# Performance work log

Hardware: AMD Instinct MI355X
Metric: run time of the kernel (lower is better)

## Reference

```python
import jax, jax.numpy as jnp
import numpy as np

TOP_K = 2


def setup_inputs() -> dict:
    key = jax.random.key(0)
    k1, k2, k3, k4, k5 = jax.random.split(key, 5)
    H, F, E = 1024, 2048, 8
    B, S = 2, 1024
    return {
        "hidden_states": jax.random.normal(k1, (B, S, H), dtype=jnp.float32),
        "gate_w": jax.random.normal(k2, (E, H), dtype=jnp.float32) * (1.0 / np.sqrt(H)),
        "w1": jax.random.normal(k3, (E, F, H), dtype=jnp.float32) * (1.0 / np.sqrt(H)),
        "w2": jax.random.normal(k4, (E, H, F), dtype=jnp.float32) * (1.0 / np.sqrt(F)),
        "w3": jax.random.normal(k5, (E, F, H), dtype=jnp.float32) * (1.0 / np.sqrt(H)),
    }


def reference(hidden_states, gate_w, w1, w2, w3):
    B, S, H = hidden_states.shape
    E = gate_w.shape[0]
    x = hidden_states.reshape(-1, H)  # [T, H]

    # Router: softmax in float32, top-k, renormalize (exact Mixtral math)
    router_logits = x @ gate_w.T  # [T, E]
    probs = jax.nn.softmax(router_logits.astype(jnp.float32), axis=-1)
    routing_weights, selected = jax.lax.top_k(probs, TOP_K)  # [T, K]
    routing_weights = routing_weights / routing_weights.sum(axis=-1, keepdims=True)
    routing_weights = routing_weights.astype(x.dtype)

    # Per-token combine weight for each expert: [T, E]
    combine = (jax.nn.one_hot(selected, E, dtype=x.dtype) * routing_weights[..., None]).sum(axis=1)

    # Dense grouped expert SwiGLU MLP (zero combine weight for unselected experts
    # makes this strictly equivalent to the gathered/dispatched computation)
    h = jnp.einsum('th,efh->etf', x, w1)   # [E, T, F]
    g = jnp.einsum('th,efh->etf', x, w3)   # [E, T, F]
    mid = jax.nn.silu(h) * g               # SwiGLU
    expert_out = jnp.einsum('etf,ehf->eth', mid, w2)  # [E, T, H]
    out = jnp.einsum('eth,te->th', expert_out, combine)  # weighted combine

    return out.reshape(B, S, H), router_logits
```

## Files before the change

### kernel.cpp

```cpp
#include <hip/hip_runtime.h>
#include <hip/hip_bf16.h>
#include <math.h>

#define H 1024
#define FF 2048
#define E 8
#define T 2048
#define NSLOT (2*T)
#define SLOT_PAD 128

#define WCONV_BLKS 12288
#define XCONV_BLKS 512
#define ROUTER_BLKS T
#define K1_BLKS (WCONV_BLKS + XCONV_BLKS + ROUTER_BLKS)

typedef __attribute__((ext_vector_type(8))) short s16x8;
typedef __attribute__((ext_vector_type(4))) float f32x4;
typedef __attribute__((ext_vector_type(4))) unsigned int u32x4;

static __device__ __forceinline__ unsigned short f2bf(float f) {
    union { float f; unsigned u; } v; v.f = f;
    unsigned r = v.u + 0x7fff + ((v.u >> 16) & 1);
    return (unsigned short)(r >> 16);
}
static __device__ __forceinline__ float bf2f(unsigned short s) {
    union { unsigned u; float f; } v; v.u = ((unsigned)s) << 16;
    return v.f;
}
static __device__ __forceinline__ unsigned pack2(float a, float b) {
    return (unsigned)f2bf(a) | ((unsigned)f2bf(b) << 16);
}

typedef __attribute__((address_space(3))) unsigned int lds_uint;
typedef const __attribute__((address_space(1))) unsigned int glob_uint;
static __device__ __forceinline__ void gl_lds16(const void* g, void* l) {
    __builtin_amdgcn_global_load_lds((glob_uint*)g, (lds_uint*)l, 16, 0, 0);
}

static __device__ __forceinline__ void expert_range(const int* __restrict__ counts,
                                                    int e, int& off, int& cnt) {
    int acc = 0;
    #pragma unroll
    for (int i = 0; i < E; ++i) {
        int c = counts[i];
        if (i < e) acc += c;
        if (i == e) cnt = c;
    }
    off = acc;
}

__global__ __launch_bounds__(256) void prep_kernel(
    const float* __restrict__ x, const float* __restrict__ gw,
    const float* __restrict__ w1, const float* __restrict__ w3,
    const float* __restrict__ w2,
    unsigned short* __restrict__ w1b, unsigned short* __restrict__ w3b,
    unsigned short* __restrict__ w2b, unsigned short* __restrict__ xb,
    float* __restrict__ logits_out, int* __restrict__ top_id,
    float* __restrict__ top_w, int* __restrict__ counts)
{
    int b = blockIdx.x;
    int tid = threadIdx.x;
    if (b < WCONV_BLKS + XCONV_BLKS) {
        const float* s; unsigned short* d; size_t i;
        if (b < WCONV_BLKS) {
            int r = b >> 12;
            s = (r == 0) ? w1 : (r == 1) ? w3 : w2;
            d = (r == 0) ? w1b : (r == 1) ? w3b : w2b;
            i = ((size_t)(b & 4095) * 256 + tid) * 16;
        } else {
            s = x; d = xb;
            i = ((size_t)(b - WCONV_BLKS) * 256 + tid) * 16;
        }
        f32x4 a0 = __builtin_nontemporal_load((const f32x4*)(s + i));
        f32x4 a1 = __builtin_nontemporal_load((const f32x4*)(s + i + 4));
        f32x4 a2 = __builtin_nontemporal_load((const f32x4*)(s + i + 8));
        f32x4 a3 = __builtin_nontemporal_load((const f32x4*)(s + i + 12));
        u32x4 r0, r1;
        r0.x = pack2(a0.x, a0.y); r0.y = pack2(a0.z, a0.w);
        r0.z = pack2(a1.x, a1.y); r0.w = pack2(a1.z, a1.w);
        r1.x = pack2(a2.x, a2.y); r1.y = pack2(a2.z, a2.w);
        r1.z = pack2(a3.x, a3.y); r1.w = pack2(a3.z, a3.w);
        *(u32x4*)(d + i) = r0;
        *(u32x4*)(d + i + 8) = r1;
        return;
    }
    int t = b - (WCONV_BLKS + XCONV_BLKS);
    int e = tid >> 5;
    int l32 = tid & 31;
    const float* xr = x + (size_t)t * H;
    const float* gr = gw + (size_t)e * H;
    float s = 0.f;
    for (int h = l32; h < H; h += 32) s += xr[h] * gr[h];
    for (int off = 16; off; off >>= 1) s += __shfl_down(s, off, 32);
    __shared__ float lg[E];
    if (l32 == 0) lg[e] = s;
    __syncthreads();
    if (tid < E) logits_out[(size_t)t * E + tid] = lg[tid];
    if (tid == 0) {
        int i1 = 0; float b1 = lg[0];
        for (int i = 1; i < E; ++i) if (lg[i] > b1) { b1 = lg[i]; i1 = i; }
        int i2 = -1; float b2 = -INFINITY;
        for (int i = 0; i < E; ++i) if (i != i1 && lg[i] > b2) { b2 = lg[i]; i2 = i; }
        float p2 = expf(b2 - b1);
        float inv = 1.f / (1.f + p2);
        top_id[2*t]   = i1;  top_id[2*t+1] = i2;
        top_w[2*t]    = inv; top_w[2*t+1]  = p2 * inv;
        atomicAdd(&counts[i1], 1);
        atomicAdd(&counts[i2], 1);
    }
}

__global__ __launch_bounds__(256) void assign_kernel(
    const int* __restrict__ top_id, const int* __restrict__ counts,
    int* __restrict__ cursors, int* __restrict__ top_pos,
    int* __restrict__ slot_token)
{
    int t = blockIdx.x * 256 + threadIdx.x;
    if (t >= T) return;
    int offs[E];
    {
        int acc = 0;
        #pragma unroll
        for (int i = 0; i < E; ++i) { offs[i] = acc; acc += counts[i]; }
    }
    #pragma unroll
    for (int k = 0; k < 2; ++k) {
        int e = top_id[2*t + k];
        int p = offs[e] + atomicAdd(&cursors[e], 1);
        top_pos[2*t + k] = p;
        slot_token[p] = t;
    }
}

__global__ __launch_bounds__(256) void gemm1_kernel(
    const unsigned short* __restrict__ xb, const int* __restrict__ slot_token,
    const unsigned short* __restrict__ w1b, const unsigned short* __restrict__ w3b,
    const int* __restrict__ counts, unsigned short* __restrict__ mid)
{
    int e = blockIdx.z;
    int off, cnt;
    expert_range(counts, e, off, cnt);
    int m0 = blockIdx.y * 128;
    if (m0 >= cnt) return;
    int f0 = blockIdx.x * 64;

    __shared__ __align__(16) unsigned short sx[128 * 64];
    __shared__ __align__(16) unsigned short s1[64 * 64];
    __shared__ __align__(16) unsigned short s3[64 * 64];

    int tid = threadIdx.x;
    int wv = tid >> 6, ln = tid & 63;
    int quad = ln >> 4, l16 = ln & 15;
    int wm = wv & 1, wn = wv >> 1;
    int xor7 = l16 & 7;

    const unsigned short* xsrc[4]; unsigned short* xdst[4];
    #pragma unroll
    for (int j = 0; j < 4; ++j) {
        int row = wv * 32 + j * 8 + (ln >> 3);
        int slot = off + m0 + row;
        if (m0 + row >= cnt) slot = off;
        int tok = slot_token[slot];
        int cl = (ln & 7) ^ (row & 7);
        xsrc[j] = xb + (size_t)tok * H + cl * 8;
        xdst[j] = &sx[(wv * 32 + j * 8) * 64];
    }
    const unsigned short *w1s[2], *w3s[2]; unsigned short *d1[2], *d3[2];
    #pragma unroll
    for (int j = 0; j < 2; ++j) {
        int row = wv * 16 + j * 8 + (ln >> 3);
        int cl = (ln & 7) ^ (row & 7);
        w1s[j] = w1b + ((size_t)e * FF + f0 + row) * H + cl * 8;
        w3s[j] = w3b + ((size_t)e * FF + f0 + row) * H + cl * 8;
        d1[j] = &s1[(wv * 16 + j * 8) * 64];
        d3[j] = &s3[(wv * 16 + j * 8) * 64];
    }

    f32x4 acc1[4][2], acc3[4][2];
    #pragma unroll
    for (int i = 0; i < 4; ++i)
        #pragma unroll
        for (int j = 0; j < 2; ++j) {
            acc1[i][j] = (f32x4){0.f, 0.f, 0.f, 0.f};
            acc3[i][j] = (f32x4){0.f, 0.f, 0.f, 0.f};
        }

    for (int k0 = 0; k0 < H; k0 += 64) {
        #pragma unroll
        for (int j = 0; j < 4; ++j) gl_lds16(xsrc[j] + k0, xdst[j]);
        #pragma unroll
        for (int j = 0; j < 2; ++j) { gl_lds16(w1s[j] + k0, d1[j]); gl_lds16(w3s[j] + k0, d3[j]); }
        __syncthreads();
        #pragma unroll
        for (int ks = 0; ks < 2; ++ks) {
            int cph = ((quad + 4 * ks) ^ xor7) << 3;
            s16x8 a[4], b1v[2], b3v[2];
            #pragma unroll
            for (int i = 0; i < 4; ++i)
                a[i] = *(const s16x8*)&sx[(wm * 64 + i * 16 + l16) * 64 + cph];
            #pragma unroll
            for (int j = 0; j < 2; ++j) {
                b1v[j] = *(const s16x8*)&s1[(wn * 32 + j * 16 + l16) * 64 + cph];
                b3v[j] = *(const s16x8*)&s3[(wn * 32 + j * 16 + l16) * 64 + cph];
            }
            #pragma unroll
            for (int i = 0; i < 4; ++i)
                #pragma unroll
                for (int j = 0; j < 2; ++j) {
                    acc1[i][j] = __builtin_amdgcn_mfma_f32_16x16x32_bf16(a[i], b1v[j], acc1[i][j], 0, 0, 0);
                    acc3[i][j] = __builtin_amdgcn_mfma_f32_16x16x32_bf16(a[i], b3v[j], acc3[i][j], 0, 0, 0);
                }
        }
        __syncthreads();
    }

    #pragma unroll
    for (int i = 0; i < 4; ++i) {
        #pragma unroll
        for (int r = 0; r < 4; ++r) {
            int row = wm * 64 + i * 16 + quad * 4 + r;
            if (m0 + row < cnt) {
                size_t base = (size_t)(off + m0 + row) * FF + f0 + wn * 32;
                #pragma unroll
                for (int j = 0; j < 2; ++j) {
                    float h = acc1[i][j][r];
                    float g = acc3[i][j][r];
                    float v = h / (1.f + __expf(-h)) * g;
                    mid[base + j * 16 + l16] = f2bf(v);
                }
            }
        }
    }
}

__global__ __launch_bounds__(256) void gemm2_kernel(
    const unsigned short* __restrict__ mid, const unsigned short* __restrict__ w2b,
    const int* __restrict__ counts, unsigned short* __restrict__ y)
{
    int e = blockIdx.z;
    int off, cnt;
    expert_range(counts, e, off, cnt);
    int m0 = blockIdx.y * 128;
    if (m0 >= cnt) return;
    int n0 = blockIdx.x * 64;

    __shared__ __align__(16) unsigned short sa[128 * 64];
    __shared__ __align__(16) unsigned short sb[64 * 64];

    int tid = threadIdx.x;
    int wv = tid >> 6, ln = tid & 63;
    int quad = ln >> 4, l16 = ln & 15;
    int wm = wv & 1, wn = wv >> 1;
    int xor7 = l16 & 7;

    const unsigned short* asrc[4]; unsigned short* adst[4];
    #pragma unroll
    for (int j = 0; j < 4; ++j) {
        int row = wv * 32 + j * 8 + (ln >> 3);
        int cl = (ln & 7) ^ (row & 7);
        asrc[j] = mid + (size_t)(off + m0 + row) * FF + cl * 8;
        adst[j] = &sa[(wv * 32 + j * 8) * 64];
    }
    const unsigned short* bsrc[2]; unsigned short* bdst[2];
    #pragma unroll
    for (int j = 0; j < 2; ++j) {
        int row = wv * 16 + j * 8 + (ln >> 3);
        int cl = (ln & 7) ^ (row & 7);
        bsrc[j] = w2b + ((size_t)e * H + n0 + row) * FF + cl * 8;
        bdst[j] = &sb[(wv * 16 + j * 8) * 64];
    }

    f32x4 acc[4][2];
    #pragma unroll
    for (int i = 0; i < 4; ++i)
        #pragma unroll
        for (int j = 0; j < 2; ++j) acc[i][j] = (f32x4){0.f, 0.f, 0.f, 0.f};

    for (int k0 = 0; k0 < FF; k0 += 64) {
        #pragma unroll
        for (int j = 0; j < 4; ++j) gl_lds16(asrc[j] + k0, adst[j]);
        #pragma unroll
        for (int j = 0; j < 2; ++j) gl_lds16(bsrc[j] + k0, bdst[j]);
        __syncthreads();
        #pragma unroll
        for (int ks = 0; ks < 2; ++ks) {
            int cph = ((quad + 4 * ks) ^ xor7) << 3;
            s16x8 a[4], b[2];
            #pragma unroll
            for (int i = 0; i < 4; ++i)
                a[i] = *(const s16x8*)&sa[(wm * 64 + i * 16 + l16) * 64 + cph];
            #pragma unroll
            for (int j = 0; j < 2; ++j)
                b[j] = *(const s16x8*)&sb[(wn * 32 + j * 16 + l16) * 64 + cph];
            #pragma unroll
            for (int i = 0; i < 4; ++i)
                #pragma unroll
                for (int j = 0; j < 2; ++j)
                    acc[i][j] = __builtin_amdgcn_mfma_f32_16x16x32_bf16(a[i], b[j], acc[i][j], 0, 0, 0);
        }
        __syncthreads();
    }

    #pragma unroll
    for (int i = 0; i < 4; ++i) {
        #pragma unroll
        for (int r = 0; r < 4; ++r) {
            int row = wm * 64 + i * 16 + quad * 4 + r;
            if (m0 + row < cnt) {
                size_t base = (size_t)(off + m0 + row) * H + n0 + wn * 32;
                #pragma unroll
                for (int j = 0; j < 2; ++j)
                    y[base + j * 16 + l16] = f2bf(acc[i][j][r]);
            }
        }
    }
}

__global__ __launch_bounds__(256) void combine_kernel(
    const unsigned short* __restrict__ y, const int* __restrict__ top_pos,
    const float* __restrict__ top_w, float* __restrict__ out)
{
    int t = blockIdx.x, tid = threadIdx.x;
    int p0 = top_pos[2*t], p1 = top_pos[2*t+1];
    float w0 = top_w[2*t], w1 = top_w[2*t+1];
    ushort4 a = ((const ushort4*)(y + (size_t)p0 * H))[tid];
    ushort4 b = ((const ushort4*)(y + (size_t)p1 * H))[tid];
    float4 o;
    o.x = w0 * bf2f(a.x) + w1 * bf2f(b.x);
    o.y = w0 * bf2f(a.y) + w1 * bf2f(b.y);
    o.z = w0 * bf2f(a.z) + w1 * bf2f(b.z);
    o.w = w0 * bf2f(a.w) + w1 * bf2f(b.w);
    ((float4*)(out + (size_t)t * H))[tid] = o;
}

extern "C" void kernel_launch(void* const* d_in, const int* in_sizes, int n_in,
                              void* d_out, int out_size, void* d_ws, size_t ws_size,
                              hipStream_t stream) {
    const float* x  = (const float*)d_in[0];
    const float* gw = (const float*)d_in[1];
    const float* w1 = (const float*)d_in[2];
    const float* w2 = (const float*)d_in[3];
    const float* w3 = (const float*)d_in[4];
    float* out    = (float*)d_out;
    float* logits = out + (size_t)T * H;

    int* counts      = (int*)d_ws;
    int* cursors     = counts + 8;
    int* top_id      = counts + 16;
    int* top_pos     = top_id + 2*T;
    int* slot_token  = top_pos + 2*T;
    float* top_w     = (float*)(slot_token + NSLOT);
    unsigned short* xb  = (unsigned short*)(top_w + 2*T);
    unsigned short* mid = xb  + (size_t)T * H;
    unsigned short* y   = mid + (size_t)(NSLOT + SLOT_PAD) * FF;
    unsigned short* w1b = y   + (size_t)NSLOT * H;
    unsigned short* w3b = w1b + (size_t)E * FF * H;
    unsigned short* w2b = w3b + (size_t)E * FF * H;

    (void)hipMemsetAsync(counts, 0, 16 * sizeof(int), stream);

    prep_kernel<<<K1_BLKS, 256, 0, stream>>>(x, gw, w1, w3, w2,
                                             w1b, w3b, w2b, xb,
                                             logits, top_id, top_w, counts);
    assign_kernel<<<(T + 255) / 256, 256, 0, stream>>>(top_id, counts, cursors,
                                                       top_pos, slot_token);
    gemm1_kernel<<<dim3(FF / 64, 16, E), 256, 0, stream>>>(xb, slot_token,
                                                           w1b, w3b, counts, mid);
    gemm2_kernel<<<dim3(H / 64, 16, E), 256, 0, stream>>>(mid, w2b, counts, y);
    combine_kernel<<<T, 256, 0, stream>>>(y, top_pos, top_w, out);
}
```

Baseline: 422.9 us.

## Interleave w1/w3 rows into one B tile and halve per-thread conversion width

The gate/up GEMM now loads w1 and w3 rows interleaved into a single 128-row LDS tile and computes one 4x4 accumulator grid. In the epilogue it pairs h and g with a lane shuffle, and only even lanes write the SwiGLU result. The weight/activation fp32-to-bf16 conversion now handles 8 elements per thread instead of 16, doubling the block count, and drops the nontemporal loads. The interleave keeps the same MFMA count but gives a uniform tile; it adds shuffles, and half the lanes sit idle during the epilogue stores.

```diff
diff --git a/kernel.cpp b/kernel.cpp
--- a/kernel.cpp
+++ b/kernel.cpp
@@ -9,8 +9,8 @@
 #define NSLOT (2*T)
 #define SLOT_PAD 128
 
-#define WCONV_BLKS 12288
-#define XCONV_BLKS 512
+#define WCONV_BLKS 24576
+#define XCONV_BLKS 1024
 #define ROUTER_BLKS T
 #define K1_BLKS (WCONV_BLKS + XCONV_BLKS + ROUTER_BLKS)
 
@@ -63,25 +63,20 @@
     if (b < WCONV_BLKS + XCONV_BLKS) {
         const float* s; unsigned short* d; size_t i;
         if (b < WCONV_BLKS) {
-            int r = b >> 12;
+            int r = b >> 13;
             s = (r == 0) ? w1 : (r == 1) ? w3 : w2;
             d = (r == 0) ? w1b : (r == 1) ? w3b : w2b;
-            i = ((size_t)(b & 4095) * 256 + tid) * 16;
+            i = ((size_t)(b & 8191) * 256 + tid) * 8;
         } else {
             s = x; d = xb;
-            i = ((size_t)(b - WCONV_BLKS) * 256 + tid) * 16;
-        }
-        f32x4 a0 = __builtin_nontemporal_load((const f32x4*)(s + i));
-        f32x4 a1 = __builtin_nontemporal_load((const f32x4*)(s + i + 4));
-        f32x4 a2 = __builtin_nontemporal_load((const f32x4*)(s + i + 8));
-        f32x4 a3 = __builtin_nontemporal_load((const f32x4*)(s + i + 12));
-        u32x4 r0, r1;
+            i = ((size_t)(b - WCONV_BLKS) * 256 + tid) * 8;
+        }
+        f32x4 a0 = *(const f32x4*)(s + i);
+        f32x4 a1 = *(const f32x4*)(s + i + 4);
+        u32x4 r0;
         r0.x = pack2(a0.x, a0.y); r0.y = pack2(a0.z, a0.w);
         r0.z = pack2(a1.x, a1.y); r0.w = pack2(a1.z, a1.w);
-        r1.x = pack2(a2.x, a2.y); r1.y = pack2(a2.z, a2.w);
-        r1.z = pack2(a3.x, a3.y); r1.w = pack2(a3.z, a3.w);
         *(u32x4*)(d + i) = r0;
-        *(u32x4*)(d + i + 8) = r1;
         return;
     }
     int t = b - (WCONV_BLKS + XCONV_BLKS);
@@ -145,8 +140,7 @@
     int f0 = blockIdx.x * 64;
 
     __shared__ __align__(16) unsigned short sx[128 * 64];
-    __shared__ __align__(16) unsigned short s1[64 * 64];
-    __shared__ __align__(16) unsigned short s3[64 * 64];
+    __shared__ __align__(16) unsigned short sb[128 * 64];
 
     int tid = threadIdx.x;
     int wv = tid >> 6, ln = tid & 63;
@@ -165,68 +159,63 @@
         xsrc[j] = xb + (size_t)tok * H + cl * 8;
         xdst[j] = &sx[(wv * 32 + j * 8) * 64];
     }
-    const unsigned short *w1s[2], *w3s[2]; unsigned short *d1[2], *d3[2];
-    #pragma unroll
-    for (int j = 0; j < 2; ++j) {
-        int row = wv * 16 + j * 8 + (ln >> 3);
+    const unsigned short* bsrc[4]; unsigned short* bdst[4];
+    #pragma unroll
+    for (int j = 0; j < 4; ++j) {
+        int row = wv * 32 + j * 8 + (ln >> 3);
+        const unsigned short* wsel = (row & 1) ? w3b : w1b;
+        int f = f0 + (row >> 1);
         int cl = (ln & 7) ^ (row & 7);
-        w1s[j] = w1b + ((size_t)e * FF + f0 + row) * H + cl * 8;
-        w3s[j] = w3b + ((size_t)e * FF + f0 + row) * H + cl * 8;
-        d1[j] = &s1[(wv * 16 + j * 8) * 64];
-        d3[j] = &s3[(wv * 16 + j * 8) * 64];
-    }
-
-    f32x4 acc1[4][2], acc3[4][2];
+        bsrc[j] = wsel + ((size_t)e * FF + f) * H + cl * 8;
+        bdst[j] = &sb[(wv * 32 + j * 8) * 64];
+    }
+
+    f32x4 acc[4][4];
     #pragma unroll
     for (int i = 0; i < 4; ++i)
         #pragma unroll
-        for (int j = 0; j < 2; ++j) {
-            acc1[i][j] = (f32x4){0.f, 0.f, 0.f, 0.f};
-            acc3[i][j] = (f32x4){0.f, 0.f, 0.f, 0.f};
-        }
+        for (int j = 0; j < 4; ++j) acc[i][j] = (f32x4){0.f, 0.f, 0.f, 0.f};
 
     for (int k0 = 0; k0 < H; k0 += 64) {
         #pragma unroll
         for (int j = 0; j < 4; ++j) gl_lds16(xsrc[j] + k0, xdst[j]);
         #pragma unroll
-        for (int j = 0; j < 2; ++j) { gl_lds16(w1s[j] + k0, d1[j]); gl_lds16(w3s[j] + k0, d3[j]); }
+        for (int j = 0; j < 4; ++j) gl_lds16(bsrc[j] + k0, bdst[j]);
         __syncthreads();
         #pragma unroll
         for (int ks = 0; ks < 2; ++ks) {
             int cph = ((quad + 4 * ks) ^ xor7) << 3;
-            s16x8 a[4], b1v[2], b3v[2];
+            s16x8 a[4], b[4];
             #pragma unroll
             for (int i = 0; i < 4; ++i)
                 a[i] = *(const s16x8*)&sx[(wm * 64 + i * 16 + l16) * 64 + cph];
             #pragma unroll
-            for (int j = 0; j < 2; ++j) {
-                b1v[j] = *(const s16x8*)&s1[(wn * 32 + j * 16 + l16) * 64 + cph];
-                b3v[j] = *(const s16x8*)&s3[(wn * 32 + j * 16 + l16) * 64 + cph];
-            }
+            for (int j = 0; j < 4; ++j)
+                b[j] = *(const s16x8*)&sb[(wn * 64 + j * 16 + l16) * 64 + cph];
             #pragma unroll
             for (int i = 0; i < 4; ++i)
                 #pragma unroll
-                for (int j = 0; j < 2; ++j) {
-                    acc1[i][j] = __builtin_amdgcn_mfma_f32_16x16x32_bf16(a[i], b1v[j], acc1[i][j], 0, 0, 0);
-                    acc3[i][j] = __builtin_amdgcn_mfma_f32_16x16x32_bf16(a[i], b3v[j], acc3[i][j], 0, 0, 0);
-                }
+                for (int j = 0; j < 4; ++j)
+                    acc[i][j] = __builtin_amdgcn_mfma_f32_16x16x32_bf16(a[i], b[j], acc[i][j], 0, 0, 0);
         }
         __syncthreads();
     }
 
+    bool evenlane = (l16 & 1) == 0;
     #pragma unroll
     for (int i = 0; i < 4; ++i) {
         #pragma unroll
         for (int r = 0; r < 4; ++r) {
             int row = wm * 64 + i * 16 + quad * 4 + r;
-            if (m0 + row < cnt) {
-                size_t base = (size_t)(off + m0 + row) * FF + f0 + wn * 32;
-                #pragma unroll
-                for (int j = 0; j < 2; ++j) {
-                    float h = acc1[i][j][r];
-                    float g = acc3[i][j][r];
-                    float v = h / (1.f + __expf(-h)) * g;
-                    mid[base + j * 16 + l16] = f2bf(v);
+            bool live = (m0 + row < cnt);
+            size_t base = (size_t)(off + m0 + row) * FF + f0 + wn * 32;
+            #pragma unroll
+            for (int j = 0; j < 4; ++j) {
+                float hv = acc[i][j][r];
+                float gv = __shfl_xor(hv, 1);
+                if (live && evenlane) {
+                    float v = hv / (1.f + __expf(-hv)) * gv;
+                    mid[base + j * 8 + (l16 >> 1)] = f2bf(v);
                 }
             }
         }
```

Result: no change. 423.5 us (+0.2%).
